# Optimization experiments

Measured on AMD Instinct MI355X. Metric: run time of the kernel, lower is better.

## Reference

```python
import jax, jax.numpy as jnp
import numpy as np

B, D = 64, 11                 # trees, tree depth
T = 2 ** D - 1                # 2047 nodes per perfect binary tree (heap layout)
H, E, L, V = 256, 256, 5, 50000
LEAF_START = 2 ** (D - 1) - 1 # first leaf index within a tree
N = B * T


def setup_inputs() -> dict:
    key = jax.random.key(0)
    ks = jax.random.split(key, 8)
    wordid = jax.random.randint(ks[0], (N, L), 0, V, dtype=jnp.int32)
    # subtoken mask: 1 for leaf nodes (which carry tokens), 0 for internal nodes
    node_is_leaf = (jnp.arange(T) >= LEAF_START).astype(jnp.int32)      # [T]
    mask = jnp.tile(node_is_leaf[:, None], (B, L))                       # [N, L]
    h0 = jnp.zeros((N, H), jnp.float32)   # init_hidden -> zeros
    c0 = jnp.zeros((N, H), jnp.float32)
    list_root_index = jnp.zeros((B,), jnp.int32)          # root at offset 0 per tree
    list_num_node = jnp.full((B,), T, dtype=jnp.int32)
    s = 0.02
    emb_table = s * jax.random.normal(ks[1], (V, E), jnp.float32)
    W_iou = s * jax.random.normal(ks[2], (3 * H, E), jnp.float32)
    U_iou = s * jax.random.normal(ks[3], (3 * H, 2 * H), jnp.float32)
    b_iou = jnp.zeros((3 * H,), jnp.float32)
    U_f_w = s * jax.random.normal(ks[4], (2 * H, 2 * H), jnp.float32)
    U_f_b = jnp.zeros((2 * H,), jnp.float32)
    return {"wordid": wordid, "mask": mask, "h0": h0, "c0": c0,
            "list_root_index": list_root_index, "list_num_node": list_num_node,
            "emb_table": emb_table, "W_iou": W_iou, "U_iou": U_iou,
            "b_iou": b_iou, "U_f_w": U_f_w, "U_f_b": U_f_b}


def reference(wordid, mask, h0, c0, list_root_index, list_num_node,
              emb_table, W_iou, U_iou, b_iou, U_f_w, U_f_b):
    fm = mask.astype(jnp.float32)
    # tree_leaf_subtoken path: embed masked ids (masked slots hit token 0, as in torch)
    emb = emb_table[wordid * mask]                # [N, L, E]
    wemb = emb.sum(axis=1)                        # [N, E]
    leaf = fm.max(axis=1)                         # [N] node-level mask
    iou0 = (wemb @ W_iou.T) * leaf[:, None]       # [N, 3H] leaf input contribution
    iou0 = iou0.reshape(B, T, 3 * H)
    c0r = c0.reshape(B, T, H)

    def apply_node(iou, c_in):
        i, o, u = jnp.split(iou + b_iou, 3, axis=-1)
        cn = jax.nn.sigmoid(i) * jnp.tanh(u) + c_in
        return jax.nn.sigmoid(o) * jnp.tanh(cn), cn

    h = jnp.zeros((B, T, H), jnp.float32)
    c = jnp.zeros((B, T, H), jnp.float32)

    # frontier 0: leaves (no in-edges -> reduce never fires, c stays c0)
    hl, cl = apply_node(iou0[:, LEAF_START:], c0r[:, LEAF_START:])
    h = h.at[:, LEAF_START:].set(hl)
    c = c.at[:, LEAF_START:].set(cl)

    # topological propagation, level by level bottom-up
    for d in range(D - 2, -1, -1):
        s, e = 2 ** d - 1, 2 ** (d + 1) - 1
        n = e - s
        # children of nodes [s,e) are contiguous at [e, e+2n) as pairs (2i+1, 2i+2)
        h_cat = h[:, e:e + 2 * n].reshape(B, n, 2 * H)
        f = jax.nn.sigmoid(h_cat @ U_f_w.T + U_f_b).reshape(B, n, 2, H)
        c_red = (f * c[:, e:e + 2 * n].reshape(B, n, 2, H)).sum(axis=2)
        iou = h_cat @ U_iou.T                     # reduce_func REPLACES iou (DGL semantics)
        hn, cn = apply_node(iou, c_red)
        h = h.at[:, s:e].set(hn)
        c = c.at[:, s:e].set(cn)

    # all trees have T nodes -> padded tree_output is just h
    tree_output = h                               # [B, T, H]
    root_h, root_c = h[:, 0], c[:, 0]             # list_root_index == 0
    return tree_output, (root_h, root_c)
```

## Files before the change

kernel.cpp:

```cpp
#include <hip/hip_runtime.h>
#include <math.h>

typedef long long i64;
typedef short short8v __attribute__((ext_vector_type(8)));
typedef float float4v __attribute__((ext_vector_type(4)));

#define Hd 256
#define Bb 64
#define Tn 2047
#define LEAF0 1023
#define NTH 33538048LL

__device__ __forceinline__ float frcp(float x){ return __builtin_amdgcn_rcpf(x); }
__device__ __forceinline__ float sigm(float x){ return frcp(1.0f+__expf(-x)); }
__device__ __forceinline__ float ftanh(float x){ return 1.0f - 2.0f*frcp(__expf(2.0f*x)+1.0f); }
__device__ __forceinline__ float bf2f(unsigned short s){
  union { unsigned u; float f; } v; v.u = ((unsigned)s)<<16; return v.f; }
__device__ __forceinline__ short f2bf(float f){
  union { float f; unsigned u; } v; v.f = f;
  unsigned r = v.u + 0x7FFF + ((v.u>>16)&1);
  return (short)(r>>16); }

#define GL2LDS(gp, lp) __builtin_amdgcn_global_load_lds( \
  (const __attribute__((address_space(1))) void*)(gp), \
  (__attribute__((address_space(3))) void*)(lp), 16, 0, 0)

__global__ __launch_bounds__(256)
void prep_kernel(const float* __restrict__ W_iou, const float* __restrict__ U_iou,
                 const float* __restrict__ U_f_w,
                 short* __restrict__ Wt2I, short* __restrict__ Wt2L,
                 const int* __restrict__ wordid, const float* __restrict__ emb,
                 short* __restrict__ hb, short* __restrict__ cbb){
  if (blockIdx.x < 320){
    int t = blockIdx.x*256 + threadIdx.x;
    int lane = t & 63, rest = t >> 6;
    int nr = rest % 20; int rest2 = rest / 20;
    int kt = rest2 & 15, hhb = rest2 >> 4;
    int g = nr/5, strip = nr - g*5;
    int j = strip*256 + hhb*64 + g*16 + (lane&15);
    int k0 = kt*32 + (lane>>4)*8;
    const float* src = (j < 768) ? (U_iou + (i64)j*512 + k0)
                                 : (U_f_w + (i64)(j-768)*512 + k0);
    short* dst = Wt2I + (i64)t*8;
    #pragma unroll
    for (int e=0;e<8;e++) dst[e] = f2bf(src[e]);
  } else if (blockIdx.x < 416){
    int t2 = (blockIdx.x-320)*256 + threadIdx.x;
    int lane = t2 & 63, rest = t2 >> 6;
    int nr = rest % 12; int rest2 = rest / 12;
    int kt = rest2 & 7, hhb = rest2 >> 3;
    int g = nr/3, strip = nr - g*3;
    int j = strip*256 + hhb*64 + g*16 + (lane&15);
    int k0 = kt*32 + (lane>>4)*8;
    const float* src = W_iou + (i64)j*256 + k0;
    short* dst = Wt2L + (i64)t2*8;
    #pragma unroll
    for (int e=0;e<8;e++) dst[e] = f2bf(src[e]);
  } else {
    int id = (blockIdx.x-416)*256 + threadIdx.x;
    int row = id >> 5, q = id & 31;
    int b = row >> 10, j = row & 1023;
    i64 tb = (i64)b*Tn;
    const int* wid = wordid + (tb + LEAF0 + j)*5;
    float s[8];
    #pragma unroll
    for (int e=0;e<8;e++) s[e] = 0.f;
    #pragma unroll
    for (int l=0;l<5;l++){
      const float* er = emb + (i64)wid[l]*Hd + q*8;
      float4 v0 = *(const float4*)(er);
      float4 v1 = *(const float4*)(er+4);
      s[0]+=v0.x; s[1]+=v0.y; s[2]+=v0.z; s[3]+=v0.w;
      s[4]+=v1.x; s[5]+=v1.y; s[6]+=v1.z; s[7]+=v1.w;
    }
    short o[8];
    #pragma unroll
    for (int e=0;e<8;e++) o[e] = f2bf(s[e]);
    short* dst = (j < 1023) ? (hb + (tb + j)*Hd) : (cbb + tb*Hd);
    *(short8v*)(dst + q*8) = *(short8v*)o;
  }
}

#define LEAF_ITER(KT, VM, BU, BL)                                            \
  {                                                                          \
    if ((KT)+2 < 8){                                                         \
      const short* bp = wbB + (i64)((KT)+2)*12*512;                          \
      _Pragma("unroll")                                                      \
      for (int s=0;s<3;s++) BL[s] = *(const short8v*)(bp + (i64)s*512);      \
    }                                                                        \
    asm volatile("" ::: "memory");                                           \
    if ((KT)+3 < 8) GL2LDS(srcA + ((KT)+3)*32, &As[((KT)+3)%5][w*512]);      \
    asm volatile("s_waitcnt vmcnt(" #VM ")" ::: "memory");                   \
    __builtin_amdgcn_s_barrier();                                            \
    asm volatile("" ::: "memory");                                           \
    short8v afr[4];                                                          \
    _Pragma("unroll")                                                        \
    for (int mr=0;mr<4;mr++)                                                 \
      afr[mr] = *(const short8v*)&As[(KT)%5][(wm*4+mr)*512 + lane*8];        \
    _Pragma("unroll")                                                        \
    for (int mr=0;mr<4;mr++)                                                 \
      _Pragma("unroll")                                                      \
      for (int s=0;s<3;s++)                                                  \
        acc[mr][s] = __builtin_amdgcn_mfma_f32_16x16x32_bf16(afr[mr], BU[s], acc[mr][s], 0, 0, 0); \
    asm volatile("s_waitcnt lgkmcnt(0)" ::: "memory");                       \
  }

__global__ __launch_bounds__(512)
void leaf_gemm(const short* __restrict__ hb, const short* __restrict__ cbb,
               const short* __restrict__ WB,
               const float* __restrict__ b_iou, const float* __restrict__ c0,
               float* __restrict__ hOut, short* __restrict__ hbOut,
               short* __restrict__ cbbOut){
  __shared__ __align__(16) short As[5][8*512];
  const int tid = threadIdx.x;
  const int lane = tid & 63, w = tid >> 6;
  const int wm = w >> 2, wg = w & 3;
  const int m0 = blockIdx.x*128;
  const int hhb = blockIdx.y;

  const int rA = m0 + w*16 + (lane&15);
  const int bA = rA >> 10, jA = rA & 1023;
  const short* baseA = (jA < 1023) ? (hb + ((i64)bA*Tn + jA)*Hd)
                                   : (cbb + (i64)bA*Tn*Hd);
  const short* srcA = baseA + (lane>>4)*8;
  const short* wbB = WB + (i64)hhb*96*512 + (i64)(wg*3)*512 + lane*8;

  float4v acc[4][3];
  #pragma unroll
  for (int mr=0;mr<4;mr++)
    #pragma unroll
    for (int s=0;s<3;s++){ float4v z = {0.f,0.f,0.f,0.f}; acc[mr][s] = z; }

  short8v b0[3], b1[3], b2[3];
  #pragma unroll
  for (int s=0;s<3;s++) b0[s] = *(const short8v*)(wbB + (i64)s*512);
  asm volatile("" ::: "memory");
  GL2LDS(srcA, &As[0][w*512]);
  GL2LDS(srcA + 32, &As[1][w*512]);
  GL2LDS(srcA + 64, &As[2][w*512]);
  asm volatile("" ::: "memory");
  #pragma unroll
  for (int s=0;s<3;s++) b1[s] = *(const short8v*)(wbB + (i64)(12+s)*512);
  asm volatile("" ::: "memory");

  LEAF_ITER(0,9,b0,b2)  LEAF_ITER(1,8,b1,b0)
  LEAF_ITER(2,9,b2,b1)  LEAF_ITER(3,9,b0,b2)
  LEAF_ITER(4,9,b1,b0)  LEAF_ITER(5,8,b2,b1)
  LEAF_ITER(6,4,b0,b2)  LEAF_ITER(7,0,b1,b0)

  const int hcol = hhb*64 + wg*16 + (lane&15);
  const float bi = b_iou[hcol], bo = b_iou[256+hcol], bu = b_iou[512+hcol];
  #pragma unroll
  for (int mr=0;mr<4;mr++){
    const int mgb = m0 + wm*64 + mr*16 + ((lane>>4)<<2);
    #pragma unroll
    for (int r=0;r<4;r++){
      const int m = mgb + r;
      const int b = m >> 10, j = m & 1023;
      const i64 n = (i64)b*Tn + LEAF0 + j;
      const float i_ = acc[mr][0][r] + bi;
      const float o_ = acc[mr][1][r] + bo;
      const float u_ = acc[mr][2][r] + bu;
      const float cn = sigm(i_)*ftanh(u_) + c0[n*Hd + hcol];
      const float hv = sigm(o_)*ftanh(cn);
      cbbOut[n*Hd + hcol] = f2bf(cn);
      hbOut[n*Hd + hcol]  = f2bf(hv);
      hOut[n*Hd + hcol] = hv;
    }
  }
}

#define LVL_ITER(KT, VM, BU, BL)                                             \
  {                                                                          \
    if ((KT)+2 < 16){                                                        \
      const short* bp = wbB + (i64)((KT)+2)*20*512;                          \
      _Pragma("unroll")                                                      \
      for (int s=0;s<5;s++) BL[s] = *(const short8v*)(bp + (i64)s*512);      \
    }                                                                        \
    asm volatile("" ::: "memory");                                           \
    if ((KT)+3 < 16) GL2LDS(srcA + ((KT)+3)*32, &As[((KT)+3)%5][w*512]);     \
    asm volatile("s_waitcnt vmcnt(" #VM ")" ::: "memory");                   \
    __builtin_amdgcn_s_barrier();                                            \
    asm volatile("" ::: "memory");                                           \
    short8v afr[4];                                                          \
    _Pragma("unroll")                                                        \
    for (int mr=0;mr<4;mr++)                                                 \
      afr[mr] = *(const short8v*)&As[(KT)%5][(wm*4+mr)*512 + lane*8];        \
    _Pragma("unroll")                                                        \
    for (int mr=0;mr<4;mr++)                                                 \
      _Pragma("unroll")                                                      \
      for (int s=0;s<5;s++)                                                  \
        acc[mr][s] = __builtin_amdgcn_mfma_f32_16x16x32_bf16(afr[mr], BU[s], acc[mr][s], 0, 0, 0); \
    asm volatile("s_waitcnt lgkmcnt(0)" ::: "memory");                       \
  }

__global__ __launch_bounds__(512)
void level_gemm(const short* __restrict__ WB,
                const float* __restrict__ b_iou, const float* __restrict__ U_f_b,
                float* __restrict__ hOut, short* __restrict__ hb, short* __restrict__ cbb,
                float* __restrict__ outRoot, int s0, int e0, int logn){
  __shared__ __align__(16) short As[5][8*512];
  const int tid = threadIdx.x;
  const int lane = tid & 63, w = tid >> 6;
  const int wm = w >> 2, wg = w & 3;
  const int m0 = blockIdx.x*128;
  const int hhb = blockIdx.y;
  const int Mtot = Bb << logn;
  const int nm1 = (1<<logn)-1;

  int rA = m0 + w*16 + (lane&15); if (rA >= Mtot) rA = Mtot-1;
  const int bA = rA >> logn, jA = rA & nm1;
  const short* srcA = hb + ((i64)bA*Tn + e0)*Hd + (i64)jA*512 + (lane>>4)*8;
  const short* wbB = WB + (i64)hhb*320*512 + (i64)(wg*5)*512 + lane*8;

  float4v acc[4][5];
  #pragma unroll
  for (int mr=0;mr<4;mr++)
    #pragma unroll
    for (int s=0;s<5;s++){ float4v z = {0.f,0.f,0.f,0.f}; acc[mr][s] = z; }

  short8v b0[5], b1[5], b2[5];
  #pragma unroll
  for (int s=0;s<5;s++) b0[s] = *(const short8v*)(wbB + (i64)s*512);
  asm volatile("" ::: "memory");
  GL2LDS(srcA, &As[0][w*512]);
  GL2LDS(srcA + 32, &As[1][w*512]);
  GL2LDS(srcA + 64, &As[2][w*512]);
  asm volatile("" ::: "memory");
  #pragma unroll
  for (int s=0;s<5;s++) b1[s] = *(const short8v*)(wbB + (i64)(20+s)*512);
  asm volatile("" ::: "memory");

  LVL_ITER( 0,13,b0,b2)  LVL_ITER( 1,12,b1,b0)  LVL_ITER( 2,13,b2,b1)
  LVL_ITER( 3,13,b0,b2)  LVL_ITER( 4,13,b1,b0)  LVL_ITER( 5,13,b2,b1)
  LVL_ITER( 6,13,b0,b2)  LVL_ITER( 7,13,b1,b0)  LVL_ITER( 8,13,b2,b1)
  LVL_ITER( 9,13,b0,b2)  LVL_ITER(10,13,b1,b0)  LVL_ITER(11,13,b2,b1)
  LVL_ITER(12,13,b0,b2)  LVL_ITER(13,12,b1,b0)  LVL_ITER(14, 6,b2,b1)
  LVL_ITER(15, 0,b0,b2)

  const int hcol = hhb*64 + wg*16 + (lane&15);
  const float bi = b_iou[hcol], bo = b_iou[256+hcol], bu = b_iou[512+hcol];
  const float bfl = U_f_b[hcol], bfr2 = U_f_b[256+hcol];
  #pragma unroll
  for (int mr=0;mr<4;mr++){
    const int mgb = m0 + wm*64 + mr*16 + ((lane>>4)<<2);
    #pragma unroll
    for (int r=0;r<4;r++){
      const int m = mgb + r;
      if (m < Mtot){
        const int b = m >> logn, j = m & nm1;
        const i64 base = (i64)b*Tn;
        const i64 cidx = (base + e0 + 2*j)*Hd + hcol;
        const float cl = bf2f((unsigned short)cbb[cidx]);
        const float cr = bf2f((unsigned short)cbb[cidx + Hd]);
        const float i_ = acc[mr][0][r]+bi, o_ = acc[mr][1][r]+bo, u_ = acc[mr][2][r]+bu;
        const float fl = acc[mr][3][r]+bfl, fr = acc[mr][4][r]+bfr2;
        const float cn = sigm(i_)*ftanh(u_) + sigm(fl)*cl + sigm(fr)*cr;
        const float hv = sigm(o_)*ftanh(cn);
        const i64 oidx = (base + s0 + j)*Hd + hcol;
        cbb[oidx] = f2bf(cn);
        hb[oidx]  = f2bf(hv);
        hOut[oidx] = hv;
        if (s0 == 0){
          outRoot[b*Hd + hcol] = hv;
          outRoot[Bb*Hd + b*Hd + hcol] = cn;
        }
      }
    }
  }
}

extern "C" void kernel_launch(void* const* d_in, const int* in_sizes, int n_in,
                              void* d_out, int out_size, void* d_ws, size_t ws_size,
                              hipStream_t stream){
  const int*   wordid = (const int*)  d_in[0];
  const float* c0     = (const float*)d_in[3];
  const float* emb    = (const float*)d_in[6];
  const float* W_iou  = (const float*)d_in[7];
  const float* U_iou  = (const float*)d_in[8];
  const float* b_iou  = (const float*)d_in[9];
  const float* U_f_w  = (const float*)d_in[10];
  const float* U_f_b  = (const float*)d_in[11];

  float* hOut    = (float*)d_out;
  float* outRoot = hOut + NTH;
  short* cbb  = (short*)d_ws;
  short* hb   = cbb + NTH;
  short* Wt2I = hb + NTH;
  short* Wt2L = Wt2I + 655360;

  hipLaunchKernelGGL(prep_kernel, dim3(8608), dim3(256), 0, stream,
                     W_iou, U_iou, U_f_w, Wt2I, Wt2L, wordid, emb, hb, cbb);
  hipLaunchKernelGGL(leaf_gemm, dim3(512,4), dim3(512), 0, stream,
                     hb, cbb, Wt2L, b_iou, c0, hOut, hb, cbb);
  for (int d = 9; d >= 0; --d){
    const int n = 1<<d, s = n-1, e = 2*n-1;
    const int bm = (64*n + 127)/128;
    hipLaunchKernelGGL(level_gemm, dim3(bm < 1 ? 1 : bm, 4), dim3(512), 0, stream,
                       Wt2I, b_iou, U_f_b, hOut, hb, cbb, outRoot, s, e, d);
  }
}
```

Measured before the change: 420.4 us.

## Fuse top six tree levels into one per-tree kernel using LDS state

Replaces the last six per-level launches (levels 5..0) with one kernel that runs one block per tree. Each block loads the level-6 h/c rows into swizzled LDS and iterates up to the root, keeping intermediate states in LDS and streaming the weights from global memory. This removes several small, low-occupancy launches and their global round trips. The level and leaf kernels also flatten the grid so the head-block index comes from the low bits of blockIdx.x, and the row bounds checks are dropped because row counts now divide evenly. The trade-off is that the fused kernel runs only 64 blocks and rereads weights from global or L2 on every level.

New measurement: 413.5 us. No clear change (-1.7%).

```diff
diff --git a/kernel.cpp b/kernel.cpp
--- a/kernel.cpp
+++ b/kernel.cpp
@@ -115,8 +115,9 @@
   const int tid = threadIdx.x;
   const int lane = tid & 63, w = tid >> 6;
   const int wm = w >> 2, wg = w & 3;
-  const int m0 = blockIdx.x*128;
-  const int hhb = blockIdx.y;
+  const int bid = blockIdx.x;
+  const int hhb = bid & 3;
+  const int m0 = (bid >> 2) * 128;
 
   const int rA = m0 + w*16 + (lane&15);
   const int bA = rA >> 10, jA = rA & 1023;
@@ -198,17 +199,17 @@
 void level_gemm(const short* __restrict__ WB,
                 const float* __restrict__ b_iou, const float* __restrict__ U_f_b,
                 float* __restrict__ hOut, short* __restrict__ hb, short* __restrict__ cbb,
-                float* __restrict__ outRoot, int s0, int e0, int logn){
+                int s0, int e0, int logn){
   __shared__ __align__(16) short As[5][8*512];
   const int tid = threadIdx.x;
   const int lane = tid & 63, w = tid >> 6;
   const int wm = w >> 2, wg = w & 3;
-  const int m0 = blockIdx.x*128;
-  const int hhb = blockIdx.y;
-  const int Mtot = Bb << logn;
+  const int bid = blockIdx.x;
+  const int hhb = bid & 3;
+  const int m0 = (bid >> 2) * 128;
   const int nm1 = (1<<logn)-1;
 
-  int rA = m0 + w*16 + (lane&15); if (rA >= Mtot) rA = Mtot-1;
+  const int rA = m0 + w*16 + (lane&15);
   const int bA = rA >> logn, jA = rA & nm1;
   const short* srcA = hb + ((i64)bA*Tn + e0)*Hd + (i64)jA*512 + (lane>>4)*8;
   const short* wbB = WB + (i64)hhb*320*512 + (i64)(wg*5)*512 + lane*8;
@@ -247,26 +248,109 @@
     #pragma unroll
     for (int r=0;r<4;r++){
       const int m = mgb + r;
-      if (m < Mtot){
-        const int b = m >> logn, j = m & nm1;
-        const i64 base = (i64)b*Tn;
-        const i64 cidx = (base + e0 + 2*j)*Hd + hcol;
-        const float cl = bf2f((unsigned short)cbb[cidx]);
-        const float cr = bf2f((unsigned short)cbb[cidx + Hd]);
-        const float i_ = acc[mr][0][r]+bi, o_ = acc[mr][1][r]+bo, u_ = acc[mr][2][r]+bu;
-        const float fl = acc[mr][3][r]+bfl, fr = acc[mr][4][r]+bfr2;
-        const float cn = sigm(i_)*ftanh(u_) + sigm(fl)*cl + sigm(fr)*cr;
-        const float hv = sigm(o_)*ftanh(cn);
-        const i64 oidx = (base + s0 + j)*Hd + hcol;
-        cbb[oidx] = f2bf(cn);
-        hb[oidx]  = f2bf(hv);
-        hOut[oidx] = hv;
-        if (s0 == 0){
-          outRoot[b*Hd + hcol] = hv;
-          outRoot[Bb*Hd + b*Hd + hcol] = cn;
+      const int b = m >> logn, j = m & nm1;
+      const i64 base = (i64)b*Tn;
+      const i64 cidx = (base + e0 + 2*j)*Hd + hcol;
+      const float cl = bf2f((unsigned short)cbb[cidx]);
+      const float cr = bf2f((unsigned short)cbb[cidx + Hd]);
+      const float i_ = acc[mr][0][r]+bi, o_ = acc[mr][1][r]+bo, u_ = acc[mr][2][r]+bu;
+      const float fl = acc[mr][3][r]+bfl, fr = acc[mr][4][r]+bfr2;
+      const float cn = sigm(i_)*ftanh(u_) + sigm(fl)*cl + sigm(fr)*cr;
+      const float hv = sigm(o_)*ftanh(cn);
+      const i64 oidx = (base + s0 + j)*Hd + hcol;
+      cbb[oidx] = f2bf(cn);
+      hb[oidx]  = f2bf(hv);
+      hOut[oidx] = hv;
+    }
+  }
+}
+
+__global__ __launch_bounds__(512)
+void tree_fused(const short* __restrict__ WB, const float* __restrict__ b_iou,
+                const float* __restrict__ U_f_b, float* __restrict__ hOut,
+                const short* __restrict__ hb, const short* __restrict__ cbb,
+                float* __restrict__ outRoot){
+  __shared__ __align__(16) char BUF[96*1024];
+  char* bAh = BUF;
+  char* bAc = BUF + 32*1024;
+  char* bBh = BUF + 64*1024;
+  char* bBc = BUF + 80*1024;
+  const int tid = threadIdx.x;
+  const int lane = tid & 63, w = tid >> 6;
+  const int hhb = w >> 1;
+  const int g0 = (w & 1) * 2;
+  const int b = blockIdx.x;
+  const i64 tb = (i64)b*Tn;
+
+  #pragma unroll
+  for (int p=0;p<4;p++){
+    int idx = p*512 + tid;
+    int row = idx >> 5, ch = idx & 31;
+    int off = row*512 + ((ch*16) ^ (((row>>1)&7)<<4));
+    *(short8v*)(bAh + off) = *(const short8v*)(hb  + (tb + 63 + row)*Hd + ch*8);
+    *(short8v*)(bAc + off) = *(const short8v*)(cbb + (tb + 63 + row)*Hd + ch*8);
+  }
+  __syncthreads();
+
+  char* inH = bAh; char* inC = bAc; char* outH = bBh; char* outC = bBc;
+
+  for (int d = 5; d >= 0; --d){
+    const int M = 1<<d, s0v = M-1;
+    const int nmf = (d == 5) ? 2 : 1;
+    for (int mf = 0; mf < nmf; ++mf){
+      const int j = mf*16 + (lane&15);
+      const int qq = lane >> 4;
+      float4v acc[2][5];
+      #pragma unroll
+      for (int c=0;c<2;c++)
+        #pragma unroll
+        for (int s=0;s<5;s++){ float4v z = {0.f,0.f,0.f,0.f}; acc[c][s] = z; }
+      #pragma unroll 2
+      for (int kt=0; kt<16; ++kt){
+        const int crow = 2*j + (kt>>3);
+        const int ccolB = ((kt&7)*32 + qq*8)*2;
+        short8v a = *(const short8v*)(inH + crow*512 + (ccolB ^ (((crow>>1)&7)<<4)));
+        const short* bp = WB + (i64)hhb*163840 + (i64)kt*10240 + (i64)lane*8;
+        #pragma unroll
+        for (int c=0;c<2;c++)
+          #pragma unroll
+          for (int s=0;s<5;s++){
+            short8v bb = *(const short8v*)(bp + (i64)((g0+c)*5+s)*512);
+            acc[c][s] = __builtin_amdgcn_mfma_f32_16x16x32_bf16(a, bb, acc[c][s], 0, 0, 0);
+          }
+      }
+      #pragma unroll
+      for (int c=0;c<2;c++){
+        const int hcol = hhb*64 + (g0+c)*16 + (lane&15);
+        const float bi = b_iou[hcol], bo = b_iou[256+hcol], bu = b_iou[512+hcol];
+        const float bfl = U_f_b[hcol], bfr2 = U_f_b[256+hcol];
+        #pragma unroll
+        for (int r=0;r<4;r++){
+          const int row = mf*16 + qq*4 + r;
+          if (row < M){
+            const int cxor = (hcol*2) ^ ((row&7)<<4);
+            const float cl = bf2f(*(const unsigned short*)(inC + row*1024 + cxor));
+            const float cr = bf2f(*(const unsigned short*)(inC + row*1024 + 512 + cxor));
+            const float i_ = acc[c][0][r]+bi, o_ = acc[c][1][r]+bo, u_ = acc[c][2][r]+bu;
+            const float fl = acc[c][3][r]+bfl, fr = acc[c][4][r]+bfr2;
+            const float cn = sigm(i_)*ftanh(u_) + sigm(fl)*cl + sigm(fr)*cr;
+            const float hv = sigm(o_)*ftanh(cn);
+            const int woff = row*512 + ((hcol*2) ^ (((row>>1)&7)<<4));
+            *(short*)(outH + woff) = f2bf(hv);
+            *(short*)(outC + woff) = f2bf(cn);
+            hOut[(tb + s0v + row)*Hd + hcol] = hv;
+            if (d == 0){
+              outRoot[b*Hd + hcol] = hv;
+              outRoot[Bb*Hd + b*Hd + hcol] = cn;
+            }
+          }
         }
       }
     }
+    __syncthreads();
+    char* t;
+    t = inH; inH = outH; outH = t;
+    t = inC; inC = outC; outC = t;
   }
 }
 
@@ -291,12 +375,13 @@
 
   hipLaunchKernelGGL(prep_kernel, dim3(8608), dim3(256), 0, stream,
                      W_iou, U_iou, U_f_w, Wt2I, Wt2L, wordid, emb, hb, cbb);
-  hipLaunchKernelGGL(leaf_gemm, dim3(512,4), dim3(512), 0, stream,
+  hipLaunchKernelGGL(leaf_gemm, dim3(2048), dim3(512), 0, stream,
                      hb, cbb, Wt2L, b_iou, c0, hOut, hb, cbb);
-  for (int d = 9; d >= 0; --d){
+  for (int d = 9; d >= 6; --d){
     const int n = 1<<d, s = n-1, e = 2*n-1;
-    const int bm = (64*n + 127)/128;
-    hipLaunchKernelGGL(level_gemm, dim3(bm < 1 ? 1 : bm, 4), dim3(512), 0, stream,
-                       Wt2I, b_iou, U_f_b, hOut, hb, cbb, outRoot, s, e, d);
-  }
-}
+    hipLaunchKernelGGL(level_gemm, dim3(2*n), dim3(512), 0, stream,
+                       Wt2I, b_iou, U_f_b, hOut, hb, cbb, s, e, d);
+  }
+  hipLaunchKernelGGL(tree_fused, dim3(64), dim3(512), 0, stream,
+                     Wt2I, b_iou, U_f_b, hOut, hb, cbb, outRoot);
+}
```
